# Performance work log

Measured on AMD Instinct MI355X. Metric: run time of the kernel, lower is better.

## Reference

```python
import math
import jax, jax.numpy as jnp
import numpy as np

L, H, C, T = 6, 16, 1024, 256   # layers, heads, n_embd, context steps (seq = 3T)
NACT, D_FF, B = 80, 4096, 4

def _conv(x, w, b, s, p):
    y = jax.lax.conv_general_dilated(x, w, (s, s), [(p, p), (p, p)],
                                     dimension_numbers=('NCHW', 'OIHW', 'NCHW'))
    return y + b[None, :, None, None]

def _ln(x, g, b):
    m = x.mean(-1, keepdims=True)
    v = ((x - m) ** 2).mean(-1, keepdims=True)
    return (x - m) / jnp.sqrt(v + 1e-5) * g + b

def _forward(states, rtgs, meta_states, circuit_feas,
             conv1_w, conv1_b, conv2_w, conv2_b, conv3_w, conv3_b,
             enc_w, enc_b, meta_w1, meta_b1, meta_w2, meta_b2,
             ret_w, ret_b, act_emb, pos_emb, gpos_emb,
             ln1_g, ln1_b, ln2_g, ln2_b,
             Wq, bq, Wk, bk, Wv, bv, Wo, bo,
             Wm1, bm1, Wm2, bm2, lnf_g, lnf_b, head_w,
             actions, timesteps):
    Bb, Tl = states.shape[0], states.shape[1]
    # state CNN encoder: (B*T, 8, 8, 10) -> 16 feats -> Linear(16, C-4)
    s = states.reshape(-1, 8, 8, 10)
    h = jax.nn.relu(_conv(s, conv1_w, conv1_b, 2, 1))
    h = jax.nn.relu(_conv(h, conv2_w, conv2_b, 2, 1))
    h = jax.nn.relu(_conv(h, conv3_w, conv3_b, 2, 1))
    se = h.reshape(h.shape[0], -1) @ enc_w + enc_b                    # (B*T, C-4)
    me = jax.nn.relu(meta_states.reshape(-1, 4) @ meta_w1 + meta_b1) @ meta_w2 + meta_b2
    state_emb = jnp.tanh(jnp.concatenate([se, me], axis=1)).reshape(Bb, Tl, C)
    # circuit embedding is computed then zeroed in source (no_circuit_emb=True) -> no effect
    rtg_emb = jnp.tanh(rtgs @ ret_w + ret_b)                          # (B, T, C)
    act_e = act_emb[actions[..., 0]]                                  # (B, T, C)
    # interleave (rtg, state, action) per timestep -> (B, 3T, C)
    tok = jnp.stack([rtg_emb, state_emb, act_e], axis=2).reshape(Bb, 3 * Tl, C)
    pos = gpos_emb[0, timesteps[:, 0, 0]][:, None, :] + pos_emb[:, :3 * Tl, :]
    x = tok + pos
    mask = jnp.tril(jnp.ones((3 * Tl, 3 * Tl), bool))
    d = C // H
    for i in range(L):
        hx = _ln(x, ln1_g[i], ln1_b[i])
        q = (hx @ Wq[i] + bq[i]).reshape(Bb, 3 * Tl, H, d)
        k = (hx @ Wk[i] + bk[i]).reshape(Bb, 3 * Tl, H, d)
        v = (hx @ Wv[i] + bv[i]).reshape(Bb, 3 * Tl, H, d)
        att = jnp.einsum('bqhd,bkhd->bhqk', q, k) / math.sqrt(d)
        att = jax.nn.softmax(jnp.where(mask, att, -jnp.inf), axis=-1)
        y = jnp.einsum('bhqk,bkhd->bqhd', att, v).reshape(Bb, 3 * Tl, C)
        x = x + (y @ Wo[i] + bo[i])
        h2 = _ln(x, ln2_g[i], ln2_b[i])
        x = x + (jax.nn.gelu(h2 @ Wm1[i] + bm1[i], approximate=False) @ Wm2[i] + bm2[i])
    logits = _ln(x, lnf_g, lnf_b) @ head_w                            # (B, 3T, NACT)
    return logits[:, 1::3, :]                                         # predictions at state tokens

def setup_inputs():
    ks = iter(jax.random.split(jax.random.key(0), 64))
    def W(*shape):
        return jax.random.normal(next(ks), shape, jnp.float32) * 0.02
    return {
        'states': jax.random.normal(next(ks), (B, T, 640), jnp.float32),
        'rtgs': jax.random.normal(next(ks), (B, T, 1), jnp.float32),
        'meta_states': jax.random.normal(next(ks), (B, T, 4), jnp.float32),
        'circuit_feas': jax.random.normal(next(ks), (B, 768), jnp.float32),
        'conv1_w': W(16, 8, 8, 8), 'conv1_b': jnp.zeros(16),
        'conv2_w': W(32, 16, 4, 4), 'conv2_b': jnp.zeros(32),
        'conv3_w': W(16, 32, 3, 3), 'conv3_b': jnp.zeros(16),
        'enc_w': W(16, C - 4), 'enc_b': jnp.zeros(C - 4),
        'meta_w1': W(4, 32), 'meta_b1': jnp.zeros(32),
        'meta_w2': W(32, 4), 'meta_b2': jnp.zeros(4),
        'ret_w': W(1, C), 'ret_b': jnp.zeros(C),
        'act_emb': W(NACT, C),
        'pos_emb': W(1, 3 * T + 1, C), 'gpos_emb': W(1, T + 1, C),
        'ln1_g': jnp.ones((L, C)), 'ln1_b': jnp.zeros((L, C)),
        'ln2_g': jnp.ones((L, C)), 'ln2_b': jnp.zeros((L, C)),
        'Wq': W(L, C, C), 'bq': jnp.zeros((L, C)),
        'Wk': W(L, C, C), 'bk': jnp.zeros((L, C)),
        'Wv': W(L, C, C), 'bv': jnp.zeros((L, C)),
        'Wo': W(L, C, C), 'bo': jnp.zeros((L, C)),
        'Wm1': W(L, C, D_FF), 'bm1': jnp.zeros((L, D_FF)),
        'Wm2': W(L, D_FF, C), 'bm2': jnp.zeros((L, C)),
        'lnf_g': jnp.ones(C), 'lnf_b': jnp.zeros(C),
        'head_w': W(C, NACT),
        'actions': jax.random.randint(next(ks), (B, T, 1), 0, NACT),
        'timesteps': jax.random.randint(next(ks), (B, 1, 1), 0, T + 1),
    }

def reference(states, rtgs, meta_states, circuit_feas,
              conv1_w, conv1_b, conv2_w, conv2_b, conv3_w, conv3_b,
              enc_w, enc_b, meta_w1, meta_b1, meta_w2, meta_b2,
              ret_w, ret_b, act_emb, pos_emb, gpos_emb,
              ln1_g, ln1_b, ln2_g, ln2_b,
              Wq, bq, Wk, bk, Wv, bv, Wo, bo,
              Wm1, bm1, Wm2, bm2, lnf_g, lnf_b, head_w,
              actions, timesteps):
    return _forward(states, rtgs, meta_states, circuit_feas,
                    conv1_w, conv1_b, conv2_w, conv2_b, conv3_w, conv3_b,
                    enc_w, enc_b, meta_w1, meta_b1, meta_w2, meta_b2,
                    ret_w, ret_b, act_emb, pos_emb, gpos_emb,
                    ln1_g, ln1_b, ln2_g, ln2_b,
                    Wq, bq, Wk, bk, Wv, bv, Wo, bo,
                    Wm1, bm1, Wm2, bm2, lnf_g, lnf_b, head_w,
                    actions, timesteps)
```

## Files before the change

### kernel.cpp

```cpp
#include <hip/hip_runtime.h>
#include <hip/hip_bf16.h>


#define S_LEN 768
#define C_DIM 1024
#define NHEAD 16
#define HDIM 64
#define BATCH 4
#define TCTX 256
#define DFF 4096
#define NACT 80
#define MROWS (BATCH * S_LEN)

typedef __attribute__((ext_vector_type(4))) float f32x4;
typedef __attribute__((ext_vector_type(8))) short bf16x8;
typedef __attribute__((ext_vector_type(8))) _Float16 f16x8;

static __device__ __forceinline__ unsigned short f2bf(float f) {
    unsigned int u = __float_as_uint(f);
    u += 0x7FFF + ((u >> 16) & 1);
    return (unsigned short)(u >> 16);
}
static __device__ __forceinline__ float bf2f(unsigned short h) {
    return __uint_as_float(((unsigned int)h) << 16);
}
static __device__ __forceinline__ unsigned short f2h(float f) {
    _Float16 h = (_Float16)f;
    return __builtin_bit_cast(unsigned short, h);
}

static __device__ __forceinline__ void gload16(void* l, const void* g) {
    __builtin_amdgcn_global_load_lds(
        (__attribute__((address_space(1))) void*)(g),
        (__attribute__((address_space(3))) void*)(l), 16, 0, 0);
}

__global__ __launch_bounds__(256) void transpose_w_kernel(
    const float* __restrict__ Wq, const float* __restrict__ Wk,
    const float* __restrict__ Wv, const float* __restrict__ Wo,
    const float* __restrict__ Wm1, const float* __restrict__ Wm2,
    unsigned short* __restrict__ Wb)
{
    const int t = blockIdx.x;
    const float* src; unsigned short* dst; int K, N, kt, nt;
    if (t < 1024) {
        const int m = t >> 8, tile = t & 255;
        src = (m == 0) ? Wq : (m == 1) ? Wk : (m == 2) ? Wv : Wo;
        dst = Wb + (size_t)m * 1048576;
        K = 1024; N = 1024; kt = tile >> 4; nt = tile & 15;
    } else if (t < 2048) {
        const int tile = t - 1024;
        src = Wm1; dst = Wb + (size_t)4 * 1048576;
        K = 1024; N = 4096; kt = tile >> 6; nt = tile & 63;
    } else {
        const int tile = t - 2048;
        src = Wm2; dst = Wb + (size_t)8 * 1048576;
        K = 4096; N = 1024; kt = tile >> 4; nt = tile & 15;
    }
    const int k0 = kt * 64, n0 = nt * 64;
    __shared__ float Ls[64][65];

    const int r = threadIdx.x >> 2, p = threadIdx.x & 3;
    #pragma unroll
    for (int i = 0; i < 4; ++i)
        *(float4*)&Ls[r][p * 16 + i * 4] =
            *(const float4*)&src[(size_t)(k0 + r) * N + n0 + p * 16 + i * 4];
    __syncthreads();

    unsigned short __align__(16) h[16];
    #pragma unroll
    for (int i = 0; i < 16; ++i) h[i] = f2bf(Ls[p * 16 + i][r]);
    unsigned short* d = dst + (size_t)(n0 + r) * K + k0 + p * 16;
    *(uint4*)d       = *(uint4*)&h[0];
    *(uint4*)(d + 8) = *(uint4*)&h[8];
}

__global__ __launch_bounds__(256) void embed_kernel(
    const float* __restrict__ states, const float* __restrict__ rtgs,
    const float* __restrict__ meta,
    const float* __restrict__ c1w, const float* __restrict__ c1b,
    const float* __restrict__ c2w, const float* __restrict__ c2b,
    const float* __restrict__ c3w, const float* __restrict__ c3b,
    const float* __restrict__ encw, const float* __restrict__ encb,
    const float* __restrict__ mw1, const float* __restrict__ mb1,
    const float* __restrict__ mw2, const float* __restrict__ mb2,
    const float* __restrict__ retw, const float* __restrict__ retb,
    const float* __restrict__ aemb, const float* __restrict__ pos,
    const float* __restrict__ gpos,
    const int* __restrict__ actions, const int* __restrict__ timesteps,
    float* __restrict__ X)
{
    const int n = blockIdx.x;
    const int b = n >> 8, t = n & 255;
    const int tid = threadIdx.x;

    __shared__ float sin_[640];
    __shared__ float h1[96];
    __shared__ float h2[32];
    __shared__ float feat[16];
    __shared__ float hidm[32];
    __shared__ float mer[4];

    for (int e = tid; e < 640; e += 256)
        sin_[e] = states[(size_t)n * 640 + e];
    __syncthreads();

    if (tid < 96) {
        int o = tid / 6, rem = tid % 6, oh = rem / 3, ow = rem % 3;
        float a = c1b[o];
        for (int ci = 0; ci < 8; ++ci)
            for (int kh = 0; kh < 8; ++kh) {
                int ih = oh * 2 - 1 + kh;
                if (ih < 0 || ih >= 8) continue;
                for (int kw = 0; kw < 8; ++kw) {
                    int iw = ow * 2 - 1 + kw;
                    if (iw < 0 || iw >= 10) continue;
                    a += c1w[((o * 8 + ci) * 8 + kh) * 8 + kw] * sin_[ci * 80 + ih * 10 + iw];
                }
            }
        h1[tid] = fmaxf(a, 0.f);
    }
    if (tid < 32) {
        float a = mb1[tid];
        for (int i = 0; i < 4; ++i)
            a += meta[(size_t)n * 4 + i] * mw1[i * 32 + tid];
        hidm[tid] = fmaxf(a, 0.f);
    }
    __syncthreads();

    if (tid < 32) {
        float a = c2b[tid];
        for (int ci = 0; ci < 16; ++ci)
            for (int kh = 0; kh < 4; ++kh) {
                int ih = -1 + kh;
                if (ih < 0 || ih >= 2) continue;
                for (int kw = 0; kw < 4; ++kw) {
                    int iw = -1 + kw;
                    if (iw < 0 || iw >= 3) continue;
                    a += c2w[((tid * 16 + ci) * 4 + kh) * 4 + kw] * h1[ci * 6 + ih * 3 + iw];
                }
            }
        h2[tid] = fmaxf(a, 0.f);
    }
    __syncthreads();

    if (tid < 16) {
        float a = c3b[tid];
        for (int ci = 0; ci < 32; ++ci)
            a += c3w[(tid * 32 + ci) * 9 + 4] * h2[ci];
        feat[tid] = fmaxf(a, 0.f);
    }
    if (tid < 4) {
        float a = mb2[tid];
        for (int j = 0; j < 32; ++j) a += hidm[j] * mw2[j * 4 + tid];
        mer[tid] = a;
    }
    __syncthreads();

    const float r = rtgs[n];
    const int a_idx = actions[n];
    const int g = timesteps[b];
    const size_t xbase = ((size_t)b * S_LEN + 3 * t) * C_DIM;

    for (int c = tid; c < C_DIM; c += 256) {
        float se;
        if (c < 1020) {
            float acc = encb[c];
            #pragma unroll
            for (int k = 0; k < 16; ++k) acc += feat[k] * encw[k * 1020 + c];
            se = acc;
        } else {
            se = mer[c - 1020];
        }
        const float st = tanhf(se);
        const float rt = tanhf(r * retw[c] + retb[c]);
        const float ae = aemb[(size_t)a_idx * C_DIM + c];
        const float gp = gpos[(size_t)g * C_DIM + c];
        X[xbase + c]             = rt + gp + pos[(size_t)(3 * t + 0) * C_DIM + c];
        X[xbase + C_DIM + c]     = st + gp + pos[(size_t)(3 * t + 1) * C_DIM + c];
        X[xbase + 2 * C_DIM + c] = ae + gp + pos[(size_t)(3 * t + 2) * C_DIM + c];
    }
}

__global__ __launch_bounds__(256) void ln_bf16_kernel(
    const float* __restrict__ in, unsigned short* __restrict__ out,
    const float* __restrict__ gw, const float* __restrict__ bw)
{
    const int row = blockIdx.x * 4 + (threadIdx.x >> 6);
    const int lane = threadIdx.x & 63;
    const float* x = in + (size_t)row * C_DIM;

    float4 v[4];
    float s = 0.f;
    #pragma unroll
    for (int j = 0; j < 4; ++j) {
        v[j] = *(const float4*)&x[lane * 4 + j * 256];
        s += (v[j].x + v[j].y) + (v[j].z + v[j].w);
    }
    #pragma unroll
    for (int o = 1; o < 64; o <<= 1) s += __shfl_xor(s, o, 64);
    const float mean = s * (1.0f / 1024.0f);

    float s2 = 0.f;
    #pragma unroll
    for (int j = 0; j < 4; ++j) {
        float dx = v[j].x - mean, dy = v[j].y - mean;
        float dz = v[j].z - mean, dw = v[j].w - mean;
        s2 += (dx * dx + dy * dy) + (dz * dz + dw * dw);
    }
    #pragma unroll
    for (int o = 1; o < 64; o <<= 1) s2 += __shfl_xor(s2, o, 64);
    const float inv = rsqrtf(s2 * (1.0f / 1024.0f) + 1e-5f);

    #pragma unroll
    for (int j = 0; j < 4; ++j) {
        const int c = lane * 4 + j * 256;
        ushort4 o4;
        o4.x = f2bf((v[j].x - mean) * inv * gw[c + 0] + bw[c + 0]);
        o4.y = f2bf((v[j].y - mean) * inv * gw[c + 1] + bw[c + 1]);
        o4.z = f2bf((v[j].z - mean) * inv * gw[c + 2] + bw[c + 2]);
        o4.w = f2bf((v[j].w - mean) * inv * gw[c + 3] + bw[c + 3]);
        *(ushort4*)&out[(size_t)row * C_DIM + c] = o4;
    }
}

__device__ __forceinline__ void gemm_core(
    const unsigned short* __restrict__ A, const unsigned short* __restrict__ Bt,
    int row0, int col0, int K, f32x4 (&acc)[4][4])
{
    __shared__ __align__(16) unsigned short As[3][4][128][8];
    __shared__ __align__(16) unsigned short Bs[3][4][128][8];

    const int tid = threadIdx.x;
    const int ar  = tid & 63, akg = tid >> 6;
    const int lane = tid & 63, w = tid >> 6;
    const int rwl = (w >> 1) * 64, cwl = (w & 1) * 64;
    const int mi = lane & 15, kg = lane >> 4;

    const unsigned short* pa = A + (size_t)(row0 + ar) * K + akg * 8;
    const unsigned short* pb = Bt + (size_t)(col0 + ar) * K + akg * 8;
    const size_t rstep = (size_t)64 * K;
    const int nk = K >> 5;

    gload16(&As[0][akg][ar][0],      pa);
    gload16(&As[0][akg][ar + 64][0], pa + rstep);
    gload16(&Bs[0][akg][ar][0],      pb);
    gload16(&Bs[0][akg][ar + 64][0], pb + rstep);
    gload16(&As[1][akg][ar][0],      pa + 32);
    gload16(&As[1][akg][ar + 64][0], pa + rstep + 32);
    gload16(&Bs[1][akg][ar][0],      pb + 32);
    gload16(&Bs[1][akg][ar + 64][0], pb + rstep + 32);

    int bsel = 0;
    for (int k = 0; k < nk; ++k) {
        if (k + 1 < nk) asm volatile("s_waitcnt vmcnt(4)" ::: "memory");
        else            asm volatile("s_waitcnt vmcnt(0)" ::: "memory");
        __builtin_amdgcn_s_barrier();
        __builtin_amdgcn_sched_barrier(0);

        if (k + 2 < nk) {
            const int b2 = (bsel >= 1) ? bsel - 1 : 2;
            const unsigned short* ga = pa + (size_t)(k + 2) * 32;
            const unsigned short* gb = pb + (size_t)(k + 2) * 32;
            gload16(&As[b2][akg][ar][0],      ga);
            gload16(&As[b2][akg][ar + 64][0], ga + rstep);
            gload16(&Bs[b2][akg][ar][0],      gb);
            gload16(&Bs[b2][akg][ar + 64][0], gb + rstep);
        }

        const unsigned short (*Ac)[128][8] = As[bsel];
        const unsigned short (*Bc)[128][8] = Bs[bsel];
        bf16x8 af[4], bfr[4];
        #pragma unroll
        for (int i = 0; i < 4; ++i) {
            af[i]  = *(const bf16x8*)&Ac[kg][rwl + i * 16 + mi][0];
            bfr[i] = *(const bf16x8*)&Bc[kg][cwl + i * 16 + mi][0];
        }
        #pragma unroll
        for (int ri = 0; ri < 4; ++ri)
            #pragma unroll
            for (int ci = 0; ci < 4; ++ci)
                acc[ri][ci] = __builtin_amdgcn_mfma_f32_16x16x32_bf16(
                    af[ri], bfr[ci], acc[ri][ci], 0, 0, 0);

        bsel = (bsel < 2) ? bsel + 1 : 0;
    }
}

template<int ACT, int OUTB, int RES>
__global__ __launch_bounds__(256) void mfma_gemm(
    const unsigned short* __restrict__ A, const unsigned short* __restrict__ Bt,
    const float* __restrict__ bias, const float* resid,
    float* outf, unsigned short* __restrict__ outb,
    int N, int K)
{
    const int row0 = blockIdx.y * 128, col0 = blockIdx.x * 128;
    f32x4 acc[4][4] = {};
    gemm_core(A, Bt, row0, col0, K, acc);

    const int lane = threadIdx.x & 63, w = threadIdx.x >> 6;
    const int rwl = (w >> 1) * 64, cwl = (w & 1) * 64;
    const int mi = lane & 15, kg = lane >> 4;

    #pragma unroll
    for (int ri = 0; ri < 4; ++ri) {
        #pragma unroll
        for (int ci = 0; ci < 4; ++ci) {
            #pragma unroll
            for (int j = 0; j < 4; ++j) {
                const int row = row0 + rwl + ri * 16 + kg * 4 + j;
                const int col = col0 + cwl + ci * 16 + mi;
                float v = acc[ri][ci][j] + bias[col];
                if (ACT) v = 0.5f * v * (1.0f + erff(v * 0.70710678118f));
                if (RES) v += resid[(size_t)row * N + col];
                if (OUTB) outb[(size_t)row * N + col] = f2bf(v);
                else      outf[(size_t)row * N + col] = v;
            }
        }
    }
}

__global__ __launch_bounds__(256) void mfma_gemm_qk(
    const unsigned short* __restrict__ A, const unsigned short* __restrict__ Wb,
    const float* __restrict__ bq, const float* __restrict__ bk,
    unsigned short* __restrict__ Qh, unsigned short* __restrict__ Kh)
{
    const int grp = blockIdx.x >> 3;
    const unsigned short* Bt = Wb + (size_t)grp * 1048576;
    const float* bias = grp == 0 ? bq : bk;
    unsigned short* out = grp == 0 ? Qh : Kh;
    const float scale = grp == 0 ? 0.125f : 1.0f;
    const int row0 = blockIdx.y * 128, col0 = (blockIdx.x & 7) * 128;

    f32x4 acc[4][4] = {};
    gemm_core(A, Bt, row0, col0, C_DIM, acc);

    const int lane = threadIdx.x & 63, w = threadIdx.x >> 6;
    const int rwl = (w >> 1) * 64, cwl = (w & 1) * 64;
    const int mi = lane & 15, kg = lane >> 4;

    #pragma unroll
    for (int ri = 0; ri < 4; ++ri)
        #pragma unroll
        for (int ci = 0; ci < 4; ++ci)
            #pragma unroll
            for (int j = 0; j < 4; ++j) {
                const int row = row0 + rwl + ri * 16 + kg * 4 + j;
                const int col = col0 + cwl + ci * 16 + mi;
                out[(size_t)row * C_DIM + col] = f2h((acc[ri][ci][j] + bias[col]) * scale);
            }
}

__global__ __launch_bounds__(256) void mfma_gemm_vt(
    const unsigned short* __restrict__ WvT, const unsigned short* __restrict__ Xb,
    const float* __restrict__ bv, unsigned short* __restrict__ Vt)
{
    const int row0 = blockIdx.y * 128, col0 = blockIdx.x * 128;
    f32x4 acc[4][4] = {};
    gemm_core(WvT, Xb, row0, col0, C_DIM, acc);

    const int lane = threadIdx.x & 63, w = threadIdx.x >> 6;
    const int rwl = (w >> 1) * 64, cwl = (w & 1) * 64;
    const int mi = lane & 15, kg = lane >> 4;

    #pragma unroll
    for (int ri = 0; ri < 4; ++ri)
        #pragma unroll
        for (int ci = 0; ci < 4; ++ci)
            #pragma unroll
            for (int j = 0; j < 4; ++j) {
                const int row = row0 + rwl + ri * 16 + kg * 4 + j;
                const int col = col0 + cwl + ci * 16 + mi;
                Vt[(size_t)row * MROWS + col] = f2h(acc[ri][ci][j] + bv[row]);
            }
}

__global__ __launch_bounds__(256) void attn_mfma(
    const unsigned short* __restrict__ Qh, const unsigned short* __restrict__ Kh,
    const unsigned short* __restrict__ Vt, unsigned short* __restrict__ Yb)
{
    const int qt = blockIdx.x, h = blockIdx.y, b = blockIdx.z;
    const int tid = threadIdx.x;
    const int lane = tid & 63, w = tid >> 6;
    const int mi = lane & 15, kg = lane >> 4;
    const int q0 = qt * 64;

    __shared__ __align__(16) char ldsraw[24576];
    unsigned short* Ks = (unsigned short*)ldsraw;
    unsigned short* Vs = (unsigned short*)(ldsraw + 8192);
    unsigned short* Ps = (unsigned short*)(ldsraw + 16384);
    float* Ob = (float*)ldsraw;

    const size_t qkbase = (size_t)b * S_LEN * C_DIM + (size_t)h * HDIM;
    const unsigned short* Kbase = Kh + qkbase;
    const unsigned short* Vbase = Vt + (size_t)h * HDIM * MROWS + (size_t)b * S_LEN;

    f16x8 QA0, QA1;
    {
        const unsigned short* qp = Qh + qkbase + (size_t)(q0 + w * 16 + mi) * C_DIM + kg * 8;
        QA0 = *(const f16x8*)qp;
        QA1 = *(const f16x8*)(qp + 32);
    }

    const int srow = tid >> 3, sc16 = tid & 7;
    const int dch = (sc16 ^ (srow & 7)) << 3;

    float mrow[4], lrow[4], alj[4];
    f32x4 Oacc[4];
    #pragma unroll
    for (int j = 0; j < 4; ++j) { mrow[j] = -1e30f; lrow[j] = 0.f; }
    #pragma unroll
    for (int df = 0; df < 4; ++df) Oacc[df] = (f32x4){0.f, 0.f, 0.f, 0.f};

    uint4 rk0, rk1, rv0, rv1;
    {
        const unsigned short* kp = Kbase + (size_t)srow * C_DIM + sc16 * 8;
        rk0 = *(const uint4*)kp;
        rk1 = *(const uint4*)(kp + (size_t)32 * C_DIM);
        const unsigned short* vp = Vbase + (size_t)srow * MROWS + sc16 * 8;
        rv0 = *(const uint4*)vp;
        rv1 = *(const uint4*)(vp + (size_t)32 * MROWS);
    }

    for (int kt = 0; kt <= qt; ++kt) {
        __syncthreads();
        *(uint4*)&Ks[srow * 64 + dch]        = rk0;
        *(uint4*)&Ks[(srow + 32) * 64 + dch] = rk1;
        *(uint4*)&Vs[srow * 64 + dch]        = rv0;
        *(uint4*)&Vs[(srow + 32) * 64 + dch] = rv1;
        if (kt < qt) {
            const unsigned short* kp = Kbase + (size_t)((kt + 1) * 64 + srow) * C_DIM + sc16 * 8;
            rk0 = *(const uint4*)kp;
            rk1 = *(const uint4*)(kp + (size_t)32 * C_DIM);
            const unsigned short* vp = Vbase + (size_t)srow * MROWS + (kt + 1) * 64 + sc16 * 8;
            rv0 = *(const uint4*)vp;
            rv1 = *(const uint4*)(vp + (size_t)32 * MROWS);
        }
        __syncthreads();

        f32x4 sa[4];
        #pragma unroll
        for (int kf = 0; kf < 4; ++kf) {
            const int key = kf * 16 + mi;
            const unsigned short* kr = Ks + key * 64;
            const f16x8 kb0 = *(const f16x8*)(kr + ((kg ^ (key & 7)) << 3));
            const f16x8 kb1 = *(const f16x8*)(kr + (((4 + kg) ^ (key & 7)) << 3));
            f32x4 z = {0.f, 0.f, 0.f, 0.f};
            z = __builtin_amdgcn_mfma_f32_16x16x32_f16(QA0, kb0, z, 0, 0, 0);
            sa[kf] = __builtin_amdgcn_mfma_f32_16x16x32_f16(QA1, kb1, z, 0, 0, 0);
        }

        if (kt == qt) {
            #pragma unroll
            for (int kf = 0; kf < 4; ++kf)
                #pragma unroll
                for (int j = 0; j < 4; ++j)
                    if (kf * 16 + mi > w * 16 + kg * 4 + j) sa[kf][j] = -1e30f;
        }

        #pragma unroll
        for (int j = 0; j < 4; ++j) {
            float rm = fmaxf(fmaxf(sa[0][j], sa[1][j]), fmaxf(sa[2][j], sa[3][j]));
            rm = fmaxf(rm, __shfl_xor(rm, 1, 16));
            rm = fmaxf(rm, __shfl_xor(rm, 2, 16));
            rm = fmaxf(rm, __shfl_xor(rm, 4, 16));
            rm = fmaxf(rm, __shfl_xor(rm, 8, 16));
            const float mn = fmaxf(mrow[j], rm);
            alj[j] = __expf(mrow[j] - mn);
            mrow[j] = mn;
            const float p0 = __expf(sa[0][j] - mn);
            const float p1 = __expf(sa[1][j] - mn);
            const float p2 = __expf(sa[2][j] - mn);
            const float p3 = __expf(sa[3][j] - mn);
            const int prow = w * 16 + kg * 4 + j;
            unsigned short* pr = Ps + prow * 64;
            const int sw = prow & 7, hi = mi >> 3, lo = mi & 7;
            pr[(((0 + hi) ^ sw) << 3) + lo] = f2h(p0);
            pr[(((2 + hi) ^ sw) << 3) + lo] = f2h(p1);
            pr[(((4 + hi) ^ sw) << 3) + lo] = f2h(p2);
            pr[(((6 + hi) ^ sw) << 3) + lo] = f2h(p3);
            float rs = p0 + p1 + p2 + p3;
            rs += __shfl_xor(rs, 1, 16);
            rs += __shfl_xor(rs, 2, 16);
            rs += __shfl_xor(rs, 4, 16);
            rs += __shfl_xor(rs, 8, 16);
            lrow[j] = lrow[j] * alj[j] + rs;
        }

        const unsigned short* pp = Ps + (w * 16 + mi) * 64;
        const int psw = mi & 7;
        const f16x8 PA0 = *(const f16x8*)(pp + ((kg ^ psw) << 3));
        const f16x8 PA1 = *(const f16x8*)(pp + (((4 + kg) ^ psw) << 3));
        #pragma unroll
        for (int df = 0; df < 4; ++df) {
            const int d = df * 16 + mi;
            const unsigned short* vr = Vs + d * 64;
            const f16x8 vb0 = *(const f16x8*)(vr + ((kg ^ (d & 7)) << 3));
            const f16x8 vb1 = *(const f16x8*)(vr + (((4 + kg) ^ (d & 7)) << 3));
            f32x4 o = Oacc[df];
            o[0] *= alj[0]; o[1] *= alj[1]; o[2] *= alj[2]; o[3] *= alj[3];
            o = __builtin_amdgcn_mfma_f32_16x16x32_f16(PA0, vb0, o, 0, 0, 0);
            Oacc[df] = __builtin_amdgcn_mfma_f32_16x16x32_f16(PA1, vb1, o, 0, 0, 0);
        }
    }

    __syncthreads();
    float inv[4];
    #pragma unroll
    for (int j = 0; j < 4; ++j) inv[j] = 1.0f / lrow[j];
    #pragma unroll
    for (int df = 0; df < 4; ++df)
        #pragma unroll
        for (int j = 0; j < 4; ++j)
            Ob[(w * 16 + kg * 4 + j) * 68 + df * 16 + mi] = Oacc[df][j] * inv[j];
    __syncthreads();

    const int orow = tid >> 2, oc0 = (tid & 3) * 16;
    unsigned short __align__(16) hx[16];
    #pragma unroll
    for (int i = 0; i < 16; ++i) hx[i] = f2bf(Ob[orow * 68 + oc0 + i]);
    unsigned short* yp = Yb + qkbase + (size_t)(q0 + orow) * C_DIM + oc0;
    *(uint4*)yp       = *(uint4*)&hx[0];
    *(uint4*)(yp + 8) = *(uint4*)&hx[8];
}

__global__ __launch_bounds__(256) void head_kernel(
    const unsigned short* __restrict__ Xb, const float* __restrict__ hw,
    float* __restrict__ out)
{
    const int n = blockIdx.x;
    const int b = n >> 8, t = n & 255;
    const int tid = threadIdx.x;
    __shared__ float rowv[C_DIM];

    const unsigned short* x = Xb + ((size_t)b * S_LEN + 3 * t + 1) * C_DIM;
    #pragma unroll
    for (int j = 0; j < 4; ++j) rowv[tid + j * 256] = bf2f(x[tid + j * 256]);
    __syncthreads();

    if (tid < NACT) {
        float a = 0.f;
        for (int k = 0; k < C_DIM; ++k) a += rowv[k] * hw[k * NACT + tid];
        out[(size_t)n * NACT + tid] = a;
    }
}

extern "C" void kernel_launch(void* const* d_in, const int* in_sizes, int n_in,
                              void* d_out, int out_size, void* d_ws, size_t ws_size,
                              hipStream_t stream) {
    const float* states  = (const float*)d_in[0];
    const float* rtgs    = (const float*)d_in[1];
    const float* meta    = (const float*)d_in[2];
    const float* c1w = (const float*)d_in[4];
    const float* c1b = (const float*)d_in[5];
    const float* c2w = (const float*)d_in[6];
    const float* c2b = (const float*)d_in[7];
    const float* c3w = (const float*)d_in[8];
    const float* c3b = (const float*)d_in[9];
    const float* encw = (const float*)d_in[10];
    const float* encb = (const float*)d_in[11];
    const float* mw1 = (const float*)d_in[12];
    const float* mb1 = (const float*)d_in[13];
    const float* mw2 = (const float*)d_in[14];
    const float* mb2 = (const float*)d_in[15];
    const float* retw = (const float*)d_in[16];
    const float* retb = (const float*)d_in[17];
    const float* aemb = (const float*)d_in[18];
    const float* pos  = (const float*)d_in[19];
    const float* gpos = (const float*)d_in[20];
    const float* ln1g = (const float*)d_in[21];
    const float* ln1b = (const float*)d_in[22];
    const float* ln2g = (const float*)d_in[23];
    const float* ln2b = (const float*)d_in[24];
    const float* Wq = (const float*)d_in[25];
    const float* bq = (const float*)d_in[26];
    const float* Wk = (const float*)d_in[27];
    const float* bk = (const float*)d_in[28];
    const float* Wv = (const float*)d_in[29];
    const float* bv = (const float*)d_in[30];
    const float* Wo = (const float*)d_in[31];
    const float* bo = (const float*)d_in[32];
    const float* Wm1 = (const float*)d_in[33];
    const float* bm1 = (const float*)d_in[34];
    const float* Wm2 = (const float*)d_in[35];
    const float* bm2 = (const float*)d_in[36];
    const float* lnfg = (const float*)d_in[37];
    const float* lnfb = (const float*)d_in[38];
    const float* hw   = (const float*)d_in[39];
    const int* actions   = (const int*)d_in[40];
    const int* timesteps = (const int*)d_in[41];

    float* out = (float*)d_out;

    char* wsc = (char*)d_ws;
    const size_t SLABB = (size_t)MROWS * C_DIM * 4;
    float* X  = (float*)wsc;
    unsigned short* Qh = (unsigned short*)(wsc + SLABB);
    unsigned short* Kh = Qh + (size_t)MROWS * C_DIM;
    unsigned short* Vt = (unsigned short*)(wsc + 2 * SLABB);
    unsigned short* Hb = (unsigned short*)(wsc + SLABB);
    unsigned short* Xb = (unsigned short*)(wsc + 4 * SLABB);
    unsigned short* Yb = (unsigned short*)(wsc + 4 * SLABB + SLABB / 2);
    unsigned short* Wb = (unsigned short*)(wsc + 5 * SLABB);

    embed_kernel<<<BATCH * TCTX, 256, 0, stream>>>(
        states, rtgs, meta, c1w, c1b, c2w, c2b, c3w, c3b, encw, encb,
        mw1, mb1, mw2, mb2, retw, retb, aemb, pos, gpos, actions, timesteps, X);

    const dim3 gqk(16, 24);
    const dim3 gvt(24, 8);
    const dim3 g1024(8, 24);
    const dim3 g4096(32, 24);
    const dim3 gattn(12, NHEAD, BATCH);

    for (int i = 0; i < 6; ++i) {
        const size_t wOff = (size_t)i * C_DIM * C_DIM;
        const size_t bOff = (size_t)i * C_DIM;
        const size_t m1Off = (size_t)i * C_DIM * DFF;

        transpose_w_kernel<<<3072, 256, 0, stream>>>(
            Wq + wOff, Wk + wOff, Wv + wOff, Wo + wOff, Wm1 + m1Off, Wm2 + m1Off, Wb);

        ln_bf16_kernel<<<MROWS / 4, 256, 0, stream>>>(X, Xb, ln1g + bOff, ln1b + bOff);
        mfma_gemm_qk<<<gqk, 256, 0, stream>>>(Xb, Wb, bq + bOff, bk + bOff, Qh, Kh);
        mfma_gemm_vt<<<gvt, 256, 0, stream>>>(Wb + (size_t)2 * 1048576, Xb, bv + bOff, Vt);
        attn_mfma<<<gattn, 256, 0, stream>>>(Qh, Kh, Vt, Yb);
        mfma_gemm<0, 0, 1><<<g1024, 256, 0, stream>>>(
            Yb, Wb + (size_t)3 * 1048576, bo + bOff, X, X, nullptr, C_DIM, C_DIM);
        ln_bf16_kernel<<<MROWS / 4, 256, 0, stream>>>(X, Xb, ln2g + bOff, ln2b + bOff);
        mfma_gemm<1, 1, 0><<<g4096, 256, 0, stream>>>(
            Xb, Wb + (size_t)4 * 1048576, bm1 + (size_t)i * DFF, nullptr, nullptr, Hb, DFF, C_DIM);
        mfma_gemm<0, 0, 1><<<g1024, 256, 0, stream>>>(
            Hb, Wb + (size_t)8 * 1048576, bm2 + bOff, X, X, nullptr, C_DIM, DFF);
    }

    ln_bf16_kernel<<<MROWS / 4, 256, 0, stream>>>(X, Xb, lnfg, lnfb);
    head_kernel<<<BATCH * TCTX, 256, 0, stream>>>(Xb, hw, out);
}
```

Measured before the change: 2.548 ms.

## Split-K residual GEMMs with atomic accumulation and unroll GEMM pipeline by three

The Wo and Wm2 projections, which previously ran as 192-block GEMMs, now use a 4-way split-K kernel that atomically adds partial sums (bias from the first split) into the fp32 residual X. This puts more blocks on the device's compute units. The GEMM main loop is also unrolled by three so the LDS buffer indices become compile-time constants. MFMA sections are wrapped in s_setprio to raise wave priority. Atomics add memory traffic and make the summation order nondeterministic. The unrolled loop assumes nk is at least 2 and follows a fixed tail pattern.

```diff
diff --git a/kernel.cpp b/kernel.cpp
--- a/kernel.cpp
+++ b/kernel.cpp
@@ -226,7 +226,7 @@
 
 __device__ __forceinline__ void gemm_core(
     const unsigned short* __restrict__ A, const unsigned short* __restrict__ Bt,
-    int row0, int col0, int K, f32x4 (&acc)[4][4])
+    int row0, int col0, int ldk, int nk, f32x4 (&acc)[4][4])
 {
     __shared__ __align__(16) unsigned short As[3][4][128][8];
     __shared__ __align__(16) unsigned short Bs[3][4][128][8];
@@ -237,10 +237,9 @@
     const int rwl = (w >> 1) * 64, cwl = (w & 1) * 64;
     const int mi = lane & 15, kg = lane >> 4;
 
-    const unsigned short* pa = A + (size_t)(row0 + ar) * K + akg * 8;
-    const unsigned short* pb = Bt + (size_t)(col0 + ar) * K + akg * 8;
-    const size_t rstep = (size_t)64 * K;
-    const int nk = K >> 5;
+    const unsigned short* pa = A + (size_t)(row0 + ar) * ldk + akg * 8;
+    const unsigned short* pb = Bt + (size_t)(col0 + ar) * ldk + akg * 8;
+    const size_t rstep = (size_t)64 * ldk;
 
     gload16(&As[0][akg][ar][0],      pa);
     gload16(&As[0][akg][ar + 64][0], pa + rstep);
@@ -251,40 +250,45 @@
     gload16(&Bs[1][akg][ar][0],      pb + 32);
     gload16(&Bs[1][akg][ar + 64][0], pb + rstep + 32);
 
-    int bsel = 0;
-    for (int k = 0; k < nk; ++k) {
-        if (k + 1 < nk) asm volatile("s_waitcnt vmcnt(4)" ::: "memory");
-        else            asm volatile("s_waitcnt vmcnt(0)" ::: "memory");
-        __builtin_amdgcn_s_barrier();
-        __builtin_amdgcn_sched_barrier(0);
-
-        if (k + 2 < nk) {
-            const int b2 = (bsel >= 1) ? bsel - 1 : 2;
-            const unsigned short* ga = pa + (size_t)(k + 2) * 32;
-            const unsigned short* gb = pb + (size_t)(k + 2) * 32;
-            gload16(&As[b2][akg][ar][0],      ga);
-            gload16(&As[b2][akg][ar + 64][0], ga + rstep);
-            gload16(&Bs[b2][akg][ar][0],      gb);
-            gload16(&Bs[b2][akg][ar + 64][0], gb + rstep);
-        }
-
-        const unsigned short (*Ac)[128][8] = As[bsel];
-        const unsigned short (*Bc)[128][8] = Bs[bsel];
-        bf16x8 af[4], bfr[4];
-        #pragma unroll
-        for (int i = 0; i < 4; ++i) {
-            af[i]  = *(const bf16x8*)&Ac[kg][rwl + i * 16 + mi][0];
-            bfr[i] = *(const bf16x8*)&Bc[kg][cwl + i * 16 + mi][0];
-        }
-        #pragma unroll
-        for (int ri = 0; ri < 4; ++ri)
-            #pragma unroll
-            for (int ci = 0; ci < 4; ++ci)
-                acc[ri][ci] = __builtin_amdgcn_mfma_f32_16x16x32_bf16(
-                    af[ri], bfr[ci], acc[ri][ci], 0, 0, 0);
-
-        bsel = (bsel < 2) ? bsel + 1 : 0;
-    }
+#define GEMM_STEP(CB, PB, KK, VM)                                          \
+    {                                                                      \
+        asm volatile("s_waitcnt vmcnt(" #VM ")" ::: "memory");             \
+        __builtin_amdgcn_s_barrier();                                      \
+        __builtin_amdgcn_sched_barrier(0);                                 \
+        if ((KK) + 2 < nk) {                                               \
+            const unsigned short* ga = pa + (size_t)((KK) + 2) * 32;       \
+            const unsigned short* gb = pb + (size_t)((KK) + 2) * 32;       \
+            gload16(&As[PB][akg][ar][0],      ga);                         \
+            gload16(&As[PB][akg][ar + 64][0], ga + rstep);                 \
+            gload16(&Bs[PB][akg][ar][0],      gb);                         \
+            gload16(&Bs[PB][akg][ar + 64][0], gb + rstep);                 \
+        }                                                                  \
+        bf16x8 af[4], bfr[4];                                              \
+        _Pragma("unroll")                                                  \
+        for (int i = 0; i < 4; ++i) {                                      \
+            af[i]  = *(const bf16x8*)&As[CB][kg][rwl + i * 16 + mi][0];    \
+            bfr[i] = *(const bf16x8*)&Bs[CB][kg][cwl + i * 16 + mi][0];    \
+        }                                                                  \
+        __builtin_amdgcn_s_setprio(1);                                     \
+        _Pragma("unroll")                                                  \
+        for (int ri = 0; ri < 4; ++ri)                                     \
+            _Pragma("unroll")                                              \
+            for (int ci = 0; ci < 4; ++ci)                                 \
+                acc[ri][ci] = __builtin_amdgcn_mfma_f32_16x16x32_bf16(     \
+                    af[ri], bfr[ci], acc[ri][ci], 0, 0, 0);                \
+        __builtin_amdgcn_s_setprio(0);                                     \
+    }
+
+    int k = 0;
+    while (k + 4 < nk) {
+        GEMM_STEP(0, 2, k,     4)
+        GEMM_STEP(1, 0, k + 1, 4)
+        GEMM_STEP(2, 1, k + 2, 4)
+        k += 3;
+    }
+    GEMM_STEP(0, 2, k,     4)
+    GEMM_STEP(1, 0, k + 1, 0)
+#undef GEMM_STEP
 }
 
 template<int ACT, int OUTB, int RES>
@@ -296,7 +300,7 @@
 {
     const int row0 = blockIdx.y * 128, col0 = blockIdx.x * 128;
     f32x4 acc[4][4] = {};
-    gemm_core(A, Bt, row0, col0, K, acc);
+    gemm_core(A, Bt, row0, col0, K, K >> 5, acc);
 
     const int lane = threadIdx.x & 63, w = threadIdx.x >> 6;
     const int rwl = (w >> 1) * 64, cwl = (w & 1) * 64;
@@ -320,6 +324,35 @@
     }
 }
 
+__global__ __launch_bounds__(256) void mfma_gemm_ressplit(
+    const unsigned short* __restrict__ A, const unsigned short* __restrict__ Bt,
+    const float* __restrict__ bias, float* __restrict__ X,
+    int N, int K)
+{
+    const int row0 = blockIdx.y * 128, col0 = blockIdx.x * 128;
+    const int ks = blockIdx.z;
+    const int kseg = K >> 2;
+    f32x4 acc[4][4] = {};
+    gemm_core(A + (size_t)ks * kseg, Bt + (size_t)ks * kseg,
+              row0, col0, K, kseg >> 5, acc);
+
+    const int lane = threadIdx.x & 63, w = threadIdx.x >> 6;
+    const int rwl = (w >> 1) * 64, cwl = (w & 1) * 64;
+    const int mi = lane & 15, kg = lane >> 4;
+
+    #pragma unroll
+    for (int ri = 0; ri < 4; ++ri)
+        #pragma unroll
+        for (int ci = 0; ci < 4; ++ci)
+            #pragma unroll
+            for (int j = 0; j < 4; ++j) {
+                const int row = row0 + rwl + ri * 16 + kg * 4 + j;
+                const int col = col0 + cwl + ci * 16 + mi;
+                float v = acc[ri][ci][j] + (ks == 0 ? bias[col] : 0.f);
+                atomicAdd(&X[(size_t)row * N + col], v);
+            }
+}
+
 __global__ __launch_bounds__(256) void mfma_gemm_qk(
     const unsigned short* __restrict__ A, const unsigned short* __restrict__ Wb,
     const float* __restrict__ bq, const float* __restrict__ bk,
@@ -333,7 +366,7 @@
     const int row0 = blockIdx.y * 128, col0 = (blockIdx.x & 7) * 128;
 
     f32x4 acc[4][4] = {};
-    gemm_core(A, Bt, row0, col0, C_DIM, acc);
+    gemm_core(A, Bt, row0, col0, C_DIM, 32, acc);
 
     const int lane = threadIdx.x & 63, w = threadIdx.x >> 6;
     const int rwl = (w >> 1) * 64, cwl = (w & 1) * 64;
@@ -357,7 +390,7 @@
 {
     const int row0 = blockIdx.y * 128, col0 = blockIdx.x * 128;
     f32x4 acc[4][4] = {};
-    gemm_core(WvT, Xb, row0, col0, C_DIM, acc);
+    gemm_core(WvT, Xb, row0, col0, C_DIM, 32, acc);
 
     const int lane = threadIdx.x & 63, w = threadIdx.x >> 6;
     const int rwl = (w >> 1) * 64, cwl = (w & 1) * 64;
@@ -609,7 +642,7 @@
 
     const dim3 gqk(16, 24);
     const dim3 gvt(24, 8);
-    const dim3 g1024(8, 24);
+    const dim3 gres(8, 24, 4);
     const dim3 g4096(32, 24);
     const dim3 gattn(12, NHEAD, BATCH);
 
@@ -625,13 +658,13 @@
         mfma_gemm_qk<<<gqk, 256, 0, stream>>>(Xb, Wb, bq + bOff, bk + bOff, Qh, Kh);
         mfma_gemm_vt<<<gvt, 256, 0, stream>>>(Wb + (size_t)2 * 1048576, Xb, bv + bOff, Vt);
         attn_mfma<<<gattn, 256, 0, stream>>>(Qh, Kh, Vt, Yb);
-        mfma_gemm<0, 0, 1><<<g1024, 256, 0, stream>>>(
-            Yb, Wb + (size_t)3 * 1048576, bo + bOff, X, X, nullptr, C_DIM, C_DIM);
+        mfma_gemm_ressplit<<<gres, 256, 0, stream>>>(
+            Yb, Wb + (size_t)3 * 1048576, bo + bOff, X, C_DIM, C_DIM);
         ln_bf16_kernel<<<MROWS / 4, 256, 0, stream>>>(X, Xb, ln2g + bOff, ln2b + bOff);
         mfma_gemm<1, 1, 0><<<g4096, 256, 0, stream>>>(
             Xb, Wb + (size_t)4 * 1048576, bm1 + (size_t)i * DFF, nullptr, nullptr, Hb, DFF, C_DIM);
-        mfma_gemm<0, 0, 1><<<g1024, 256, 0, stream>>>(
-            Hb, Wb + (size_t)8 * 1048576, bm2 + bOff, X, X, nullptr, C_DIM, DFF);
+        mfma_gemm_ressplit<<<gres, 256, 0, stream>>>(
+            Hb, Wb + (size_t)8 * 1048576, bm2 + bOff, X, C_DIM, DFF);
     }
 
     ln_bf16_kernel<<<MROWS / 4, 256, 0, stream>>>(X, Xb, lnfg, lnfb);
```

Result: faster. 2.459 ms (-3.5%).
